# Kernel tuning notes

Measured on AMD Instinct MI355X. Metric: run time of the kernel, lower is better.

The kernel has to match this reference:

```python
import jax, jax.numpy as jnp
import numpy as np

B, N, IN_DIM, OUT_DIM = 16, 2048, 512, 512

def _xavier(key, shape):
    bound = float(np.sqrt(6.0 / (shape[0] + shape[1])))
    return jax.random.uniform(key, shape, jnp.float32, -bound, bound)

def setup_inputs() -> dict:
    key = jax.random.key(0)
    kx, kk, kq, kv = jax.random.split(key, 4)
    return {
        "x": jax.random.normal(kx, (B, N, IN_DIM), jnp.float32),
        "W_key": _xavier(kk, (IN_DIM, OUT_DIM)),
        "W_query": _xavier(kq, (IN_DIM, OUT_DIM)),
        "W_value": _xavier(kv, (IN_DIM, OUT_DIM)),
    }

def reference(x, W_key, W_query, W_value):
    # projections: [B, N, out_dim]
    k = jnp.matmul(x, W_key)
    q = jnp.matmul(x, W_query)
    v = jnp.matmul(x, W_value)
    scale = jnp.sqrt(jnp.asarray(IN_DIM, jnp.float32))
    scores = jnp.einsum("bnd,bmd->bnm", q, k) / scale  # [B, N, N]
    weights = jax.nn.softmax(scores, axis=2)
    attn = jnp.einsum("bnm,bmd->bnd", weights, v)  # [B, N, out_dim]
    return jnp.mean(attn, axis=1)  # [B, out_dim]
```

## Files before the change

### kernel.cpp

```cpp
#include <hip/hip_runtime.h>
#include <hip/hip_bf16.h>
#include <hip/hip_fp16.h>
#include <stdint.h>

#define NB 16
#define NN 2048
#define ND 512
#define SSCALE 0.044194173824159216f

typedef unsigned short u16;
typedef unsigned int u32;
typedef float f32x4 __attribute__((ext_vector_type(4)));
typedef __bf16 bf16x8 __attribute__((ext_vector_type(8)));
typedef unsigned short u16x8 __attribute__((ext_vector_type(8)));

__device__ __forceinline__ float bf2f(u16 h) {
  union { u32 u; float f; } v; v.u = ((u32)h) << 16; return v.f;
}
__device__ __forceinline__ u16 f2bf(float f) {
  union { float f; u32 u; } v; v.f = f;
  u32 r = v.u + 0x7fffu + ((v.u >> 16) & 1u);
  return (u16)(r >> 16);
}
__device__ __forceinline__ u16 f2h(float f) {
  __half h = __float2half(f);
  union { __half h; u16 u; } v; v.h = h; return v.u;
}
__device__ __forceinline__ float h2f(u16 u) {
  union { u16 u; __half h; } v; v.u = u; return __half2float(v.h);
}

__device__ __forceinline__ void async16(const void* g, void* l) {
  __builtin_amdgcn_global_load_lds(
      (const __attribute__((address_space(1))) u32*)g,
      (__attribute__((address_space(3))) u32*)l,
      16, 0, 0);
}

#define TP 136

template <int MODE, bool AF32>
__global__ __launch_bounds__(256, 2) void gemm_bt(
    const void* __restrict__ Av, const u16* __restrict__ B, u16* __restrict__ C,
    float* __restrict__ Lrow, int lda, int ldb, int ldc, int K,
    long long sA, long long sB, long long sC, float cscale) {
  const int tid  = threadIdx.x;
  const int w    = tid >> 6;
  const int lane = tid & 63;
  const int wm   = w >> 1, wn = w & 1;
  const int lrow = lane & 15, quad = lane >> 4;
  const long long z = blockIdx.z;

  const float* Abf = (const float*)Av + z * sA + (size_t)blockIdx.y * 128 * lda;
  const u16*   Abh = (const u16*)Av   + z * sA + (size_t)blockIdx.y * 128 * lda;
  const u16*   Bb  = B + z * sB + (size_t)blockIdx.x * 128 * ldb;

  __shared__ __align__(16) union {
    struct { u16 a[128 * 32]; u16 b[128 * 32]; } st;
    u16 tile[128 * TP];
  } sm;

  f32x4 acc[4][4];
#pragma unroll
  for (int i = 0; i < 4; i++)
#pragma unroll
    for (int j = 0; j < 4; j++) acc[i][j] = (f32x4){0.f, 0.f, 0.f, 0.f};

  for (int k0 = 0; k0 < K; k0 += 32) {
    if (k0) __syncthreads();
    if (AF32) {
      u16x8 va[2];
#pragma unroll
      for (int t = 0; t < 2; t++) {
        int ch  = t * 256 + tid;
        int row = ch >> 2;
        int cc  = (ch & 3) * 8;
        const float4* p = (const float4*)(Abf + (size_t)row * lda + k0 + cc);
        float4 f0 = p[0], f1 = p[1];
        u16x8 r;
        r[0] = f2bf(f0.x); r[1] = f2bf(f0.y); r[2] = f2bf(f0.z); r[3] = f2bf(f0.w);
        r[4] = f2bf(f1.x); r[5] = f2bf(f1.y); r[6] = f2bf(f1.z); r[7] = f2bf(f1.w);
        va[t] = r;
        async16(Bb + (size_t)row * ldb + k0 + cc, &sm.st.b[ch * 8]);
      }
#pragma unroll
      for (int t = 0; t < 2; t++) *(u16x8*)&sm.st.a[(t * 256 + tid) * 8] = va[t];
    } else {
#pragma unroll
      for (int t = 0; t < 2; t++) {
        int ch  = t * 256 + tid;
        int row = ch >> 2;
        int cc  = (ch & 3) * 8;
        async16(Abh + (size_t)row * lda + k0 + cc, &sm.st.a[ch * 8]);
        async16(Bb  + (size_t)row * ldb + k0 + cc, &sm.st.b[ch * 8]);
      }
    }
    __syncthreads();

    bf16x8 af[4], bfr[4];
#pragma unroll
    for (int i = 0; i < 4; i++) {
      af[i]  = *(const bf16x8*)&sm.st.a[(wm * 64 + i * 16 + lrow) * 32 + quad * 8];
      bfr[i] = *(const bf16x8*)&sm.st.b[(wn * 64 + i * 16 + lrow) * 32 + quad * 8];
    }
#pragma unroll
    for (int i = 0; i < 4; i++)
#pragma unroll
      for (int j = 0; j < 4; j++)
        acc[i][j] =
            __builtin_amdgcn_mfma_f32_16x16x32_bf16(af[i], bfr[j], acc[i][j], 0, 0, 0);
  }

  __syncthreads();

  if (MODE == 0) {
#pragma unroll
    for (int i = 0; i < 4; i++)
#pragma unroll
      for (int j = 0; j < 4; j++)
#pragma unroll
        for (int r = 0; r < 4; r++) {
          int row = wm * 64 + i * 16 + quad * 4 + r;
          int col = wn * 64 + j * 16 + lrow;
          sm.tile[row * TP + col] = f2bf(acc[i][j][r] * cscale);
        }
  } else {
    float* Lb = Lrow + z * NN + (size_t)blockIdx.y * 128;
#pragma unroll
    for (int i = 0; i < 4; i++)
#pragma unroll
      for (int r = 0; r < 4; r++) {
        int row = wm * 64 + i * 16 + quad * 4 + r;
        float rs = 0.f;
#pragma unroll
        for (int j = 0; j < 4; j++) {
          int col = wn * 64 + j * 16 + lrow;
          float e = __expf(fminf(acc[i][j][r] * cscale, 10.f));
          sm.tile[row * TP + col] = f2h(e);
          rs += e;
        }
        rs += __shfl_xor(rs, 1); rs += __shfl_xor(rs, 2);
        rs += __shfl_xor(rs, 4); rs += __shfl_xor(rs, 8);
        if (lrow == 0) atomicAdd(&Lb[row], rs);
      }
  }
  __syncthreads();

  u16* Cb = C + z * sC + (size_t)blockIdx.y * 128 * ldc + (size_t)blockIdx.x * 128;
#pragma unroll
  for (int s = 0; s < 8; s++) {
    int flat = s * 2048 + tid * 8;
    int row = flat >> 7, col = flat & 127;
    *(u16x8*)(Cb + (size_t)row * ldc + col) = *(const u16x8*)&sm.tile[row * TP + col];
  }
}

__global__ void cast_f32_bf16(const float* __restrict__ x, u16* __restrict__ xb) {
  size_t i = ((size_t)blockIdx.x * 256 + threadIdx.x) * 8;
  float4 f0 = *(const float4*)(x + i);
  float4 f1 = *(const float4*)(x + i + 4);
  u16x8 r;
  r[0] = f2bf(f0.x); r[1] = f2bf(f0.y); r[2] = f2bf(f0.z); r[3] = f2bf(f0.w);
  r[4] = f2bf(f1.x); r[5] = f2bf(f1.y); r[6] = f2bf(f1.z); r[7] = f2bf(f1.w);
  *(u16x8*)(xb + i) = r;
}

__global__ void col_sum(const __half* __restrict__ E, const float* __restrict__ L,
                        float* __restrict__ c) {
  int m8 = threadIdx.x * 8;
  int n0 = blockIdx.y * 128;
  int z  = blockIdx.z;
  const u16* Ep = (const u16*)E + ((size_t)z * NN + n0) * NN + m8;
  const float* lp = L + (size_t)z * NN + n0;
  float a[8];
#pragma unroll
  for (int k = 0; k < 8; k++) a[k] = 0.f;
#pragma unroll 2
  for (int n = 0; n < 128; n++) {
    u16x8 h = *(const u16x8*)(Ep + (size_t)n * NN);
    float il = 1.0f / lp[n];
#pragma unroll
    for (int k = 0; k < 8; k++) a[k] += h2f(h[k]) * il;
  }
  float* cp = c + (size_t)z * NN + m8;
#pragma unroll
  for (int k = 0; k < 8; k++) atomicAdd(&cp[k], a[k]);
}

__global__ void tx_accum(const u16* __restrict__ xb, const float* __restrict__ c,
                         float* __restrict__ t) {
  int b = blockIdx.x, mc = blockIdx.y, d = threadIdx.x;
  const u16* vp = xb + ((size_t)b * NN + mc * 128) * ND;
  const float* cp = c + b * NN + mc * 128;
  float a0 = 0.f, a1 = 0.f;
#pragma unroll 4
  for (int m = 0; m < 128; m++) {
    float cm = cp[m];
    a0 += cm * bf2f(vp[(size_t)m * ND + d]);
    a1 += cm * bf2f(vp[(size_t)m * ND + 256 + d]);
  }
  atomicAdd(&t[b * ND + d], a0);
  atomicAdd(&t[b * ND + 256 + d], a1);
}

__global__ void final_wv(const float* __restrict__ t, const float* __restrict__ Wv,
                         float* __restrict__ out) {
  int b = blockIdx.x, d = blockIdx.y * 256 + threadIdx.x;
  const float* tb = t + b * ND;
  float a = 0.f;
#pragma unroll 4
  for (int l = 0; l < ND; l++) a += tb[l] * Wv[(size_t)l * ND + d];
  out[b * ND + d] = a * (1.f / (float)NN);
}

extern "C" void kernel_launch(void* const* d_in, const int* in_sizes, int n_in,
                              void* d_out, int out_size, void* d_ws, size_t ws_size,
                              hipStream_t stream) {
  const float* x  = (const float*)d_in[0];
  const float* Wk = (const float*)d_in[1];
  const float* Wq = (const float*)d_in[2];
  const float* Wv = (const float*)d_in[3];
  float* out = (float*)d_out;

  char* ws = (char*)d_ws;
  size_t off = 0;
  float* L   = (float*)(ws + off); off += (size_t)NB * NN * 4;
  float* c   = (float*)(ws + off); off += (size_t)NB * NN * 4;
  float* t   = (float*)(ws + off); off += (size_t)NB * ND * 4;
  u16* Wqb   = (u16*)(ws + off);   off += (size_t)ND * ND * 2;
  u16* Mt    = (u16*)(ws + off);   off += (size_t)ND * ND * 2;
  const size_t small_total = off;

  const size_t XBSZ = (size_t)NB * NN * ND * 2;
  const size_t SB1  = (size_t)NN * NN * 2;
  u16* xb   = (u16*)(ws + small_total);
  u16* y    = (u16*)(ws + small_total + XBSZ);
  __half* E = (__half*)(ws + small_total + 2 * XBSZ);
  size_t srem = ws_size > small_total + 2 * XBSZ
              ? ws_size - small_total - 2 * XBSZ : 0;
  int chb = 0, sr = 128;
  if      (srem >= 16 * SB1) chb = 16;
  else if (srem >=  8 * SB1) chb = 8;
  else if (srem >=  4 * SB1) chb = 4;
  else if (srem >=  2 * SB1) chb = 2;
  else if (srem >=  1 * SB1) chb = 1;
  else {
    if      (srem >= (size_t)1024 * NN * 2) sr = 1024;
    else if (srem >= (size_t)512  * NN * 2) sr = 512;
    else if (srem >= (size_t)256  * NN * 2) sr = 256;
  }

  (void)hipMemsetAsync(L, 0, (size_t)(2 * NB * NN + NB * ND) * sizeof(float),
                       stream);

  cast_f32_bf16<<<8192, 256, 0, stream>>>(x, xb);
  cast_f32_bf16<<<128, 256, 0, stream>>>(Wq, Wqb);

  gemm_bt<0, true><<<dim3(4, 4, 1), 256, 0, stream>>>(
      Wk, Wqb, Mt, nullptr, ND, ND, ND, ND, 0, 0, 0, SSCALE);

  gemm_bt<0, false><<<dim3(4, 256, 1), 256, 0, stream>>>(
      xb, Mt, y, nullptr, ND, ND, ND, ND, 0, 0, 0, 1.0f);

  const long long sR = (long long)NN * ND;
  const long long sS = (long long)NN * NN;

  if (chb >= 1) {
    for (int cc = 0; cc < NB / chb; ++cc) {
      size_t o = (size_t)cc * chb * NN;
      gemm_bt<1, false><<<dim3(16, 16, chb), 256, 0, stream>>>(
          y + o * ND, xb + o * ND, (u16*)E, L + o, ND, ND, NN, ND,
          sR, sR, sS, 1.0f);
      col_sum<<<dim3(1, 16, chb), 256, 0, stream>>>(E, L + o, c + o);
    }
  } else {
    for (int b = 0; b < NB; ++b) {
      for (int ch = 0; ch < NN / sr; ++ch) {
        size_t o = (size_t)b * NN + (size_t)ch * sr;
        gemm_bt<1, false><<<dim3(16, sr / 128, 1), 256, 0, stream>>>(
            y + o * ND, xb + (size_t)b * NN * ND, (u16*)E, L + o,
            ND, ND, NN, ND, 0, 0, 0, 1.0f);
        col_sum<<<dim3(1, sr / 128, 1), 256, 0, stream>>>(E, L + o, c + b * NN);
      }
    }
  }

  tx_accum<<<dim3(NB, 16), 256, 0, stream>>>(xb, c, t);
  final_wv<<<dim3(NB, 2), 256, 0, stream>>>(t, Wv, out);
  (void)in_sizes; (void)n_in; (void)out_size;
}
```

Baseline: 364.0 us.

## Fuse output reduction kernels, read fp32 Wq directly, split col_sum finer

The small Wk·Wq GEMM now converts the fp32 B operand in-kernel, which removes a separate cast launch and its buffer. col_sum now uses 32-row blocks, giving four times as many blocks. tx_accum and final_wv are merged into one kernel per batch that reduces over all 2048 rows and then applies Wv from shared memory. This drops atomics and a launch, but the fused kernel runs only 16 blocks over a 32MB read, so it risks being latency-bound with low parallelism.

Measured after the change: 469.1 us. +28.9%, slower.

```diff
diff --git a/kernel.cpp b/kernel.cpp
--- a/kernel.cpp
+++ b/kernel.cpp
@@ -39,9 +39,9 @@
 
 #define TP 136
 
-template <int MODE, bool AF32>
+template <int MODE, bool AF32, bool BF32>
 __global__ __launch_bounds__(256, 2) void gemm_bt(
-    const void* __restrict__ Av, const u16* __restrict__ B, u16* __restrict__ C,
+    const void* __restrict__ Av, const void* __restrict__ Bv, u16* __restrict__ C,
     float* __restrict__ Lrow, int lda, int ldb, int ldc, int K,
     long long sA, long long sB, long long sC, float cscale) {
   const int tid  = threadIdx.x;
@@ -53,7 +53,8 @@
 
   const float* Abf = (const float*)Av + z * sA + (size_t)blockIdx.y * 128 * lda;
   const u16*   Abh = (const u16*)Av   + z * sA + (size_t)blockIdx.y * 128 * lda;
-  const u16*   Bb  = B + z * sB + (size_t)blockIdx.x * 128 * ldb;
+  const float* Bbf = (const float*)Bv + z * sB + (size_t)blockIdx.x * 128 * ldb;
+  const u16*   Bbh = (const u16*)Bv   + z * sB + (size_t)blockIdx.x * 128 * ldb;
 
   __shared__ __align__(16) union {
     struct { u16 a[128 * 32]; u16 b[128 * 32]; } st;
@@ -68,32 +69,38 @@
 
   for (int k0 = 0; k0 < K; k0 += 32) {
     if (k0) __syncthreads();
-    if (AF32) {
-      u16x8 va[2];
-#pragma unroll
-      for (int t = 0; t < 2; t++) {
-        int ch  = t * 256 + tid;
-        int row = ch >> 2;
-        int cc  = (ch & 3) * 8;
+    u16x8 va[2], vb[2];
+#pragma unroll
+    for (int t = 0; t < 2; t++) {
+      int ch  = t * 256 + tid;
+      int row = ch >> 2;
+      int cc  = (ch & 3) * 8;
+      if (AF32) {
         const float4* p = (const float4*)(Abf + (size_t)row * lda + k0 + cc);
         float4 f0 = p[0], f1 = p[1];
         u16x8 r;
         r[0] = f2bf(f0.x); r[1] = f2bf(f0.y); r[2] = f2bf(f0.z); r[3] = f2bf(f0.w);
         r[4] = f2bf(f1.x); r[5] = f2bf(f1.y); r[6] = f2bf(f1.z); r[7] = f2bf(f1.w);
         va[t] = r;
-        async16(Bb + (size_t)row * ldb + k0 + cc, &sm.st.b[ch * 8]);
-      }
-#pragma unroll
-      for (int t = 0; t < 2; t++) *(u16x8*)&sm.st.a[(t * 256 + tid) * 8] = va[t];
-    } else {
-#pragma unroll
-      for (int t = 0; t < 2; t++) {
-        int ch  = t * 256 + tid;
-        int row = ch >> 2;
-        int cc  = (ch & 3) * 8;
+      } else {
         async16(Abh + (size_t)row * lda + k0 + cc, &sm.st.a[ch * 8]);
-        async16(Bb  + (size_t)row * ldb + k0 + cc, &sm.st.b[ch * 8]);
-      }
+      }
+      if (BF32) {
+        const float4* p = (const float4*)(Bbf + (size_t)row * ldb + k0 + cc);
+        float4 f0 = p[0], f1 = p[1];
+        u16x8 r;
+        r[0] = f2bf(f0.x); r[1] = f2bf(f0.y); r[2] = f2bf(f0.z); r[3] = f2bf(f0.w);
+        r[4] = f2bf(f1.x); r[5] = f2bf(f1.y); r[6] = f2bf(f1.z); r[7] = f2bf(f1.w);
+        vb[t] = r;
+      } else {
+        async16(Bbh + (size_t)row * ldb + k0 + cc, &sm.st.b[ch * 8]);
+      }
+    }
+#pragma unroll
+    for (int t = 0; t < 2; t++) {
+      int ch = t * 256 + tid;
+      if (AF32) *(u16x8*)&sm.st.a[ch * 8] = va[t];
+      if (BF32) *(u16x8*)&sm.st.b[ch * 8] = vb[t];
     }
     __syncthreads();
 
@@ -168,15 +175,15 @@
 __global__ void col_sum(const __half* __restrict__ E, const float* __restrict__ L,
                         float* __restrict__ c) {
   int m8 = threadIdx.x * 8;
-  int n0 = blockIdx.y * 128;
+  int n0 = blockIdx.y * 32;
   int z  = blockIdx.z;
   const u16* Ep = (const u16*)E + ((size_t)z * NN + n0) * NN + m8;
   const float* lp = L + (size_t)z * NN + n0;
   float a[8];
 #pragma unroll
   for (int k = 0; k < 8; k++) a[k] = 0.f;
-#pragma unroll 2
-  for (int n = 0; n < 128; n++) {
+#pragma unroll 4
+  for (int n = 0; n < 32; n++) {
     u16x8 h = *(const u16x8*)(Ep + (size_t)n * NN);
     float il = 1.0f / lp[n];
 #pragma unroll
@@ -187,30 +194,30 @@
   for (int k = 0; k < 8; k++) atomicAdd(&cp[k], a[k]);
 }
 
-__global__ void tx_accum(const u16* __restrict__ xb, const float* __restrict__ c,
-                         float* __restrict__ t) {
-  int b = blockIdx.x, mc = blockIdx.y, d = threadIdx.x;
-  const u16* vp = xb + ((size_t)b * NN + mc * 128) * ND;
-  const float* cp = c + b * NN + mc * 128;
+__global__ void out_fused(const u16* __restrict__ xb, const float* __restrict__ c,
+                          const float* __restrict__ Wv, float* __restrict__ out) {
+  int b = blockIdx.x, d = threadIdx.x;
+  __shared__ float tl[ND];
+  const u16* vp = xb + (size_t)b * NN * ND;
+  const float* cp = c + b * NN;
   float a0 = 0.f, a1 = 0.f;
-#pragma unroll 4
-  for (int m = 0; m < 128; m++) {
+#pragma unroll 8
+  for (int m = 0; m < NN; m++) {
     float cm = cp[m];
     a0 += cm * bf2f(vp[(size_t)m * ND + d]);
     a1 += cm * bf2f(vp[(size_t)m * ND + 256 + d]);
   }
-  atomicAdd(&t[b * ND + d], a0);
-  atomicAdd(&t[b * ND + 256 + d], a1);
-}
-
-__global__ void final_wv(const float* __restrict__ t, const float* __restrict__ Wv,
-                         float* __restrict__ out) {
-  int b = blockIdx.x, d = blockIdx.y * 256 + threadIdx.x;
-  const float* tb = t + b * ND;
-  float a = 0.f;
+  tl[d] = a0; tl[d + 256] = a1;
+  __syncthreads();
+  float o0 = 0.f, o1 = 0.f;
 #pragma unroll 4
-  for (int l = 0; l < ND; l++) a += tb[l] * Wv[(size_t)l * ND + d];
-  out[b * ND + d] = a * (1.f / (float)NN);
+  for (int l = 0; l < ND; l++) {
+    float t = tl[l];
+    o0 += t * Wv[(size_t)l * ND + d];
+    o1 += t * Wv[(size_t)l * ND + 256 + d];
+  }
+  out[b * ND + d] = o0 * (1.f / (float)NN);
+  out[b * ND + 256 + d] = o1 * (1.f / (float)NN);
 }
 
 extern "C" void kernel_launch(void* const* d_in, const int* in_sizes, int n_in,
@@ -226,8 +233,6 @@
   size_t off = 0;
   float* L   = (float*)(ws + off); off += (size_t)NB * NN * 4;
   float* c   = (float*)(ws + off); off += (size_t)NB * NN * 4;
-  float* t   = (float*)(ws + off); off += (size_t)NB * ND * 4;
-  u16* Wqb   = (u16*)(ws + off);   off += (size_t)ND * ND * 2;
   u16* Mt    = (u16*)(ws + off);   off += (size_t)ND * ND * 2;
   const size_t small_total = off;
 
@@ -250,16 +255,14 @@
     else if (srem >= (size_t)256  * NN * 2) sr = 256;
   }
 
-  (void)hipMemsetAsync(L, 0, (size_t)(2 * NB * NN + NB * ND) * sizeof(float),
-                       stream);
+  (void)hipMemsetAsync(L, 0, (size_t)(2 * NB * NN) * sizeof(float), stream);
 
   cast_f32_bf16<<<8192, 256, 0, stream>>>(x, xb);
-  cast_f32_bf16<<<128, 256, 0, stream>>>(Wq, Wqb);
-
-  gemm_bt<0, true><<<dim3(4, 4, 1), 256, 0, stream>>>(
-      Wk, Wqb, Mt, nullptr, ND, ND, ND, ND, 0, 0, 0, SSCALE);
-
-  gemm_bt<0, false><<<dim3(4, 256, 1), 256, 0, stream>>>(
+
+  gemm_bt<0, true, true><<<dim3(4, 4, 1), 256, 0, stream>>>(
+      Wk, Wq, Mt, nullptr, ND, ND, ND, ND, 0, 0, 0, SSCALE);
+
+  gemm_bt<0, false, false><<<dim3(4, 256, 1), 256, 0, stream>>>(
       xb, Mt, y, nullptr, ND, ND, ND, ND, 0, 0, 0, 1.0f);
 
   const long long sR = (long long)NN * ND;
@@ -268,24 +271,23 @@
   if (chb >= 1) {
     for (int cc = 0; cc < NB / chb; ++cc) {
       size_t o = (size_t)cc * chb * NN;
-      gemm_bt<1, false><<<dim3(16, 16, chb), 256, 0, stream>>>(
+      gemm_bt<1, false, false><<<dim3(16, 16, chb), 256, 0, stream>>>(
           y + o * ND, xb + o * ND, (u16*)E, L + o, ND, ND, NN, ND,
           sR, sR, sS, 1.0f);
-      col_sum<<<dim3(1, 16, chb), 256, 0, stream>>>(E, L + o, c + o);
+      col_sum<<<dim3(1, 64, chb), 256, 0, stream>>>(E, L + o, c + o);
     }
   } else {
     for (int b = 0; b < NB; ++b) {
       for (int ch = 0; ch < NN / sr; ++ch) {
         size_t o = (size_t)b * NN + (size_t)ch * sr;
-        gemm_bt<1, false><<<dim3(16, sr / 128, 1), 256, 0, stream>>>(
+        gemm_bt<1, false, false><<<dim3(16, sr / 128, 1), 256, 0, stream>>>(
             y + o * ND, xb + (size_t)b * NN * ND, (u16*)E, L + o,
             ND, ND, NN, ND, 0, 0, 0, 1.0f);
-        col_sum<<<dim3(1, sr / 128, 1), 256, 0, stream>>>(E, L + o, c + b * NN);
-      }
-    }
-  }
-
-  tx_accum<<<dim3(NB, 16), 256, 0, stream>>>(xb, c, t);
-  final_wv<<<dim3(NB, 2), 256, 0, stream>>>(t, Wv, out);
+        col_sum<<<dim3(1, sr / 32, 1), 256, 0, stream>>>(E, L + o, c + b * NN);
+      }
+    }
+  }
+
+  out_fused<<<NB, 256, 0, stream>>>(xb, c, Wv, out);
   (void)in_sizes; (void)n_in; (void)out_size;
 }
```
